# Performance work log

Measured on AMD Instinct MI355X. Metric: run time of the kernel, lower is better.

## Reference

```python
import jax, jax.numpy as jnp
import numpy as np
from jax import lax

B, C_IN, C_OUT, N, R, K = 16, 64, 64, 32768, 32, 3
GROUPS, GN_EPS = 8, 1e-5


def swish(x):
    return x * jax.nn.sigmoid(x)


def group_norm(x, gamma, beta):
    b, c = x.shape[:2]
    xg = x.reshape(b, GROUPS, -1)
    mu = xg.mean(-1, keepdims=True)
    var = xg.var(-1, keepdims=True)
    xn = ((xg - mu) * lax.rsqrt(var + GN_EPS)).reshape(x.shape)
    shp = (1, c) + (1,) * (x.ndim - 2)
    return xn * gamma.reshape(shp) + beta.reshape(shp)


def conv3d(x, w, b):
    y = lax.conv_general_dilated(x, w, (1, 1, 1), 'SAME',
                                 dimension_numbers=('NCDHW', 'OIDHW', 'NCDHW'))
    return y + b.reshape(1, -1, 1, 1, 1)


def voxelize(features, coords):
    # features [B,C,N], coords [B,3,N] -> vox [B,C,R,R,R], norm_coords [B,3,N] in [0,R-1]
    c = coords - coords.mean(axis=2, keepdims=True)
    scale = jnp.linalg.norm(c, axis=1, keepdims=True).max(axis=2, keepdims=True) * 2.0  # eps=0
    norm = jnp.clip((c / scale + 0.5) * R, 0.0, R - 1)
    vc = jnp.round(norm).astype(jnp.int32)
    idx = (vc[:, 0] * R + vc[:, 1]) * R + vc[:, 2]  # [B,N] flat voxel index

    def per_batch(f, i):  # f [C,N], i [N] -> [C, R^3] scatter-average
        sums = jax.ops.segment_sum(f.T, i, num_segments=R ** 3)  # [R^3, C]
        cnt = jax.ops.segment_sum(jnp.ones(i.shape, f.dtype), i, num_segments=R ** 3)
        return (sums / jnp.maximum(cnt, 1.0)[:, None]).T

    vox = jax.vmap(per_batch)(features, idx).reshape(features.shape[0], features.shape[1], R, R, R)
    return vox, norm


def trilinear_devoxelize(vox, coords):
    # vox [B,C,R,R,R], coords [B,3,N] float in [0,R-1] -> [B,C,N]
    b, c = vox.shape[:2]
    flat = vox.reshape(b, c, R ** 3)
    c0f = jnp.floor(coords)
    f = coords - c0f
    i0 = jnp.clip(c0f.astype(jnp.int32), 0, R - 1)
    i1 = jnp.clip(i0 + 1, 0, R - 1)
    out = jnp.zeros((b, c, coords.shape[2]), vox.dtype)
    for xi, wx in ((i0[:, 0], 1.0 - f[:, 0]), (i1[:, 0], f[:, 0])):
        for yi, wy in ((i0[:, 1], 1.0 - f[:, 1]), (i1[:, 1], f[:, 1])):
            for zi, wz in ((i0[:, 2], 1.0 - f[:, 2]), (i1[:, 2], f[:, 2])):
                idx = (xi * R + yi) * R + zi  # [B,N]
                w = (wx * wy * wz)[:, None, :]
                out = out + jnp.take_along_axis(flat, idx[:, None, :], axis=2) * w
    return out


def setup_inputs():
    key = jax.random.key(0)
    ks = jax.random.split(key, 6)
    s1 = 1.0 / np.sqrt(C_IN * K ** 3)
    s2 = 1.0 / np.sqrt(C_OUT * K ** 3)
    sp = 1.0 / np.sqrt(C_IN)
    return {
        'features': jax.random.normal(ks[0], (B, C_IN, N), jnp.float32),
        'coords': jax.random.normal(ks[1], (B, 3, N), jnp.float32),
        'w1': jax.random.normal(ks[2], (C_OUT, C_IN, K, K, K), jnp.float32) * s1,
        'b1': jnp.zeros((C_OUT,), jnp.float32),
        'g1': jnp.ones((C_OUT,), jnp.float32),
        'be1': jnp.zeros((C_OUT,), jnp.float32),
        'w2': jax.random.normal(ks[3], (C_OUT, C_OUT, K, K, K), jnp.float32) * s2,
        'b2': jnp.zeros((C_OUT,), jnp.float32),
        'g2': jnp.ones((C_OUT,), jnp.float32),
        'be2': jnp.zeros((C_OUT,), jnp.float32),
        'wp': jax.random.normal(ks[4], (C_OUT, C_IN), jnp.float32) * sp,
        'bp': jnp.zeros((C_OUT,), jnp.float32),
        'gp': jnp.ones((C_OUT,), jnp.float32),
        'bep': jnp.zeros((C_OUT,), jnp.float32),
    }


def reference(features, coords, w1, b1, g1, be1, w2, b2, g2, be2, wp, bp, gp, bep):
    coords_sg = lax.stop_gradient(coords)  # torch: coords.detach() inside Voxelization
    vox, norm_coords = voxelize(features, coords_sg)
    h = swish(group_norm(conv3d(vox, w1, b1), g1, be1))
    # Dropout(0.1) is identity in eval mode
    h = swish(group_norm(conv3d(h, w2, b2), g2, be2))
    vpts = trilinear_devoxelize(h, norm_coords)
    pf = swish(group_norm(jnp.einsum('oc,bcn->bon', wp, features) + bp[None, :, None], gp, bep))
    return (vpts + pf, coords)
```

## Files before the change

kernel.cpp:

```cpp
#include <hip/hip_runtime.h>
#include <hip/hip_bf16.h>
#include <math.h>

#define BB   16
#define CCH  64
#define NPT  32768
#define RR   32
#define R3   32768
#define GSZ  262144
#define VOXB 2228224

typedef __attribute__((ext_vector_type(8))) short bfx8;
typedef __attribute__((ext_vector_type(8))) unsigned short usx8;
typedef __attribute__((ext_vector_type(16))) float f32x16;

__device__ __forceinline__ short f2bf(float f) {
    unsigned u = __builtin_bit_cast(unsigned, f);
    u += 0x7fff + ((u >> 16) & 1);
    return (short)(u >> 16);
}
__device__ __forceinline__ float bf2f(unsigned short s) {
    unsigned u = ((unsigned)s) << 16;
    return __builtin_bit_cast(float, u);
}

__device__ __forceinline__ float blockReduceSumF(float v) {
    __shared__ float sm[16];
    #pragma unroll
    for (int o = 32; o > 0; o >>= 1) v += __shfl_down(v, o);
    __syncthreads();
    if ((threadIdx.x & 63) == 0) sm[threadIdx.x >> 6] = v;
    __syncthreads();
    float s = 0.f;
    int nw = blockDim.x >> 6;
    for (int i = 0; i < nw; ++i) s += sm[i];
    return s;
}

__device__ __forceinline__ float blockReduceMaxF(float v) {
    __shared__ float sm[16];
    #pragma unroll
    for (int o = 32; o > 0; o >>= 1) v = fmaxf(v, __shfl_down(v, o));
    __syncthreads();
    if ((threadIdx.x & 63) == 0) sm[threadIdx.x >> 6] = v;
    __syncthreads();
    float s = sm[0];
    int nw = blockDim.x >> 6;
    for (int i = 1; i < nw; ++i) s = fmaxf(s, sm[i]);
    return s;
}

__global__ void k_cstat_sum(const float* __restrict__ coords, float* __restrict__ csum) {
    int b = blockIdx.x >> 3, seg = blockIdx.x & 7;
    const float* cb = coords + (size_t)b * 3 * NPT;
    int n0 = seg << 12;
    float sx = 0.f, sy = 0.f, sz = 0.f;
    for (int n = n0 + threadIdx.x; n < n0 + 4096; n += 256) {
        sx += cb[n]; sy += cb[NPT + n]; sz += cb[2 * NPT + n];
    }
    sx = blockReduceSumF(sx);
    sy = blockReduceSumF(sy);
    sz = blockReduceSumF(sz);
    if (threadIdx.x == 0) {
        atomicAdd(&csum[b * 4 + 0], sx);
        atomicAdd(&csum[b * 4 + 1], sy);
        atomicAdd(&csum[b * 4 + 2], sz);
    }
}

__global__ void k_cstat_max(const float* __restrict__ coords, const float* __restrict__ csum,
                            int* __restrict__ cmax) {
    int b = blockIdx.x >> 3, seg = blockIdx.x & 7;
    const float* cb = coords + (size_t)b * 3 * NPT;
    float mx = csum[b * 4 + 0] * (1.f / NPT);
    float my = csum[b * 4 + 1] * (1.f / NPT);
    float mz = csum[b * 4 + 2] * (1.f / NPT);
    int n0 = seg << 12;
    float mn = 0.f;
    for (int n = n0 + threadIdx.x; n < n0 + 4096; n += 256) {
        float x = cb[n] - mx, y = cb[NPT + n] - my, z = cb[2 * NPT + n] - mz;
        mn = fmaxf(mn, sqrtf(x * x + y * y + z * z));
    }
    mn = blockReduceMaxF(mn);
    if (threadIdx.x == 0) atomicMax(&cmax[b], __float_as_int(mn));
}

__global__ void k_norm_idx(const float* __restrict__ coords, const float* __restrict__ csum,
                           const int* __restrict__ cmax,
                           float* __restrict__ normc, int* __restrict__ vidx,
                           int* __restrict__ hist, float* __restrict__ out2) {
    int t = blockIdx.x * 256 + threadIdx.x;
    int b = t >> 15, n = t & 32767;
    float mx = csum[b * 4 + 0] * (1.f / NPT);
    float my = csum[b * 4 + 1] * (1.f / NPT);
    float mz = csum[b * 4 + 2] * (1.f / NPT);
    float scale = 2.f * __int_as_float(cmax[b]);
    const float* cb = coords + (size_t)b * 3 * NPT;
    float x = cb[n], y = cb[NPT + n], z = cb[2 * NPT + n];
    float nx = fminf(fmaxf(((x - mx) / scale + 0.5f) * 32.f, 0.f), 31.f);
    float ny = fminf(fmaxf(((y - my) / scale + 0.5f) * 32.f, 0.f), 31.f);
    float nz = fminf(fmaxf(((z - mz) / scale + 0.5f) * 32.f, 0.f), 31.f);
    float* nb = normc + (size_t)b * 3 * NPT;
    nb[n] = nx; nb[NPT + n] = ny; nb[2 * NPT + n] = nz;
    int vx = (int)rintf(nx), vy = (int)rintf(ny), vz = (int)rintf(nz);
    int v = (vx * 32 + vy) * 32 + vz;
    vidx[t] = v;
    atomicAdd(&hist[(b << 15) + v], 1);
    float* o2 = out2 + (size_t)b * 3 * NPT;
    o2[n] = x; o2[NPT + n] = y; o2[2 * NPT + n] = z;
}

__global__ __launch_bounds__(1024) void k_prefix(const int* __restrict__ hist,
                                                 int* __restrict__ startB,
                                                 int* __restrict__ base) {
    int b = blockIdx.x;
    int tid = threadIdx.x;
    const int* h = hist + (b << 15);
    int loc[32];
    int s = 0;
    #pragma unroll
    for (int j = 0; j < 32; ++j) { loc[j] = h[tid * 32 + j]; s += loc[j]; }
    __shared__ int sm[1024];
    sm[tid] = s;
    __syncthreads();
    for (int o = 1; o < 1024; o <<= 1) {
        int v = (tid >= o) ? sm[tid - o] : 0;
        __syncthreads();
        sm[tid] += v;
        __syncthreads();
    }
    int run = (tid ? sm[tid - 1] : 0);
    #pragma unroll
    for (int j = 0; j < 32; ++j) {
        int idx = (b << 15) + tid * 32 + j;
        startB[idx] = run;
        base[idx] = run;
        run += loc[j];
    }
}

__global__ __launch_bounds__(256) void k_reorder(const float* __restrict__ feat,
                                                 const int* __restrict__ vidx,
                                                 int* __restrict__ base,
                                                 short* __restrict__ featT) {
    __shared__ float tile[64][65];
    __shared__ int sslot[64];
    int blk = blockIdx.x;
    int b = blk >> 9;
    int n0 = (blk & 511) << 6;
    int tid = threadIdx.x;
    const float* fb = feat + ((size_t)b << 21);
    for (int e = tid; e < 64 * 64; e += 256) {
        int c = e >> 6, nn = e & 63;
        tile[c][nn] = fb[((size_t)c << 15) + n0 + nn];
    }
    if (tid < 64) {
        int v = vidx[(b << 15) + n0 + tid];
        sslot[tid] = atomicAdd(&base[(b << 15) + v], 1);
    }
    __syncthreads();
    int p = tid >> 2, q = tid & 3;
    int slot = sslot[p];
    short* dst = featT + (((size_t)((b << 15) + slot)) << 6) + q * 16;
    unsigned pk[8];
    #pragma unroll
    for (int k = 0; k < 8; ++k) {
        unsigned lo16 = (unsigned short)f2bf(tile[q * 16 + 2 * k][p]);
        unsigned hi16 = (unsigned short)f2bf(tile[q * 16 + 2 * k + 1][p]);
        pk[k] = lo16 | (hi16 << 16);
    }
    *(int4*)dst = make_int4(pk[0], pk[1], pk[2], pk[3]);
    *(int4*)(dst + 8) = make_int4(pk[4], pk[5], pk[6], pk[7]);
}

__global__ void k_vox_accum(const short* __restrict__ featT, const int* __restrict__ startB,
                            const int* __restrict__ base, short* __restrict__ vout) {
    int t = blockIdx.x * 256 + threadIdx.x;
    int lane4 = t & 15;
    int v = (t >> 4) & 32767;
    int b = t >> 19;
    int start = startB[(b << 15) + v];
    int end   = base[(b << 15) + v];
    float4 acc = make_float4(0.f, 0.f, 0.f, 0.f);
    const short* fT = featT + (((size_t)b << 15) << 6) + lane4 * 4;
    for (int p = start; p < end; ++p) {
        short4 hv = *(const short4*)(fT + ((size_t)p << 6));
        acc.x += bf2f((unsigned short)hv.x);
        acc.y += bf2f((unsigned short)hv.y);
        acc.z += bf2f((unsigned short)hv.z);
        acc.w += bf2f((unsigned short)hv.w);
    }
    float rc = 1.f / fmaxf((float)(end - start), 1.f);
    short4 pk;
    pk.x = f2bf(acc.x * rc); pk.y = f2bf(acc.y * rc);
    pk.z = f2bf(acc.z * rc); pk.w = f2bf(acc.w * rc);
    *(short4*)(vout + (size_t)b * VOXB + ((size_t)(v >> 5) * 34 + (v & 31) + 1) * 64 + lane4 * 4) = pk;
}

__global__ void k_padzero(short* __restrict__ v) {
    int t = blockIdx.x * 256 + threadIdx.x;
    int q = t & 7, zp = (t >> 3) & 1, xy = (t >> 4) & 1023, b = t >> 14;
    int z = zp ? 33 : 0;
    *(int4*)(v + (size_t)b * VOXB + ((size_t)xy * 34 + z) * 64 + q * 8) = make_int4(0, 0, 0, 0);
}

__global__ void k_wprep(const float* __restrict__ w, short* __restrict__ wT) {
    int e = blockIdx.x * 256 + threadIdx.x;
    int ci = e & 63, co = (e >> 6) & 63, k = e >> 12;
    wT[e] = f2bf(w[(size_t)(co * 64 + ci) * 27 + k]);
}

__global__ __launch_bounds__(256, 2) void k_conv_mfma(
    const short* __restrict__ vin, const short* __restrict__ wT,
    const float* __restrict__ bias, short* __restrict__ vout, float* __restrict__ st)
{
    __shared__ short lds[36 * 1088];
    __shared__ float sred[8][2];
    int bid = blockIdx.x;
    int xcd = bid & 7, sub = bid >> 3;
    int b = (xcd << 1) | (sub >> 6);
    int tile = sub & 63;
    int x0 = (tile >> 3) << 2, y0 = (tile & 7) << 2;
    int tid = threadIdx.x;
    int wv = tid >> 6, l = tid & 63;
    int lo = l & 31, hi = l >> 5;
    const short* vb = vin + (size_t)b * VOXB;
    int xo = x0 + wv;
    if (tid < 16) ((float*)sred)[tid] = 0.f;

    f32x16 acc[2][4];
    #pragma unroll
    for (int cb = 0; cb < 2; ++cb)
        #pragma unroll
        for (int j = 0; j < 4; ++j)
            #pragma unroll
            for (int i = 0; i < 16; ++i) acc[cb][j][i] = 0.f;

    #pragma unroll
    for (int h = 0; h < 2; ++h) {
        if (h) __syncthreads();
        for (int e = tid; e < 4896; e += 256) {
            int line = e / 136, r = e - line * 136;
            int z = r >> 2, q = r & 3;
            int xx = line / 6, yy = line - xx * 6;
            int xi = x0 + xx - 1, yi = y0 + yy - 1;
            int4 v = make_int4(0, 0, 0, 0);
            if ((unsigned)xi < 32u && (unsigned)yi < 32u)
                v = *(const int4*)(vb + ((size_t)(xi * 32 + yi) * 34 + z) * 64 + h * 32 + q * 8);
            int dst = line * 1088 + z * 32 + ((q * 8) ^ ((z & 3) << 3));
            *(int4*)(lds + dst) = v;
        }
        __syncthreads();
        const short* wbase = wT + lo * 64 + h * 32 + hi * 8;
        #pragma unroll
        for (int dx = 0; dx < 3; ++dx) {
            const short* ldsx = lds + ((wv + dx) * 6) * 1088;
            #pragma unroll
            for (int dz = 0; dz < 3; ++dz) {
                int zz = lo + dz;
                int swz = (zz & 3) << 3;
                const short* bcol = ldsx + zz * 32;
                #pragma unroll
                for (int s = 0; s < 2; ++s) {
                    int slot = (s * 16 + hi * 8) ^ swz;
                    const short* wt0 = wbase + (dx * 9 + dz) * 4096 + s * 16;
                    bfx8 wA0 = *(const bfx8*)(wt0);
                    bfx8 wB0 = *(const bfx8*)(wt0 + 2048);
                    bfx8 wA1 = *(const bfx8*)(wt0 + 3 * 4096);
                    bfx8 wB1 = *(const bfx8*)(wt0 + 3 * 4096 + 2048);
                    bfx8 wA2 = *(const bfx8*)(wt0 + 6 * 4096);
                    bfx8 wB2 = *(const bfx8*)(wt0 + 6 * 4096 + 2048);
                    #pragma unroll
                    for (int L = 0; L < 6; ++L) {
                        bfx8 bv = *(const bfx8*)(bcol + L * 1088 + slot);
                        if (L <= 3) {
                            acc[0][L] = __builtin_amdgcn_mfma_f32_32x32x16_bf16(wA0, bv, acc[0][L], 0, 0, 0);
                            acc[1][L] = __builtin_amdgcn_mfma_f32_32x32x16_bf16(wB0, bv, acc[1][L], 0, 0, 0);
                        }
                        if (L >= 1 && L <= 4) {
                            acc[0][L-1] = __builtin_amdgcn_mfma_f32_32x32x16_bf16(wA1, bv, acc[0][L-1], 0, 0, 0);
                            acc[1][L-1] = __builtin_amdgcn_mfma_f32_32x32x16_bf16(wB1, bv, acc[1][L-1], 0, 0, 0);
                        }
                        if (L >= 2) {
                            acc[0][L-2] = __builtin_amdgcn_mfma_f32_32x32x16_bf16(wA2, bv, acc[0][L-2], 0, 0, 0);
                            acc[1][L-2] = __builtin_amdgcn_mfma_f32_32x32x16_bf16(wB2, bv, acc[1][L-2], 0, 0, 0);
                        }
                    }
                }
            }
        }
    }

    float gs[8], gs2[8];
    #pragma unroll
    for (int g = 0; g < 8; ++g) { gs[g] = 0.f; gs2[g] = 0.f; }
    short* ob = vout + (size_t)b * VOXB;
    #pragma unroll
    for (int cb = 0; cb < 2; ++cb) {
        #pragma unroll
        for (int j = 0; j < 4; ++j) {
            size_t rb = ((size_t)(xo * 32 + y0 + j) * 34 + 1 + lo) * 64;
            #pragma unroll
            for (int q = 0; q < 4; ++q) {
                int co0 = cb * 32 + hi * 4 + q * 8;
                float v0 = acc[cb][j][q * 4 + 0] + bias[co0 + 0];
                float v1 = acc[cb][j][q * 4 + 1] + bias[co0 + 1];
                float v2 = acc[cb][j][q * 4 + 2] + bias[co0 + 2];
                float v3 = acc[cb][j][q * 4 + 3] + bias[co0 + 3];
                int g = cb * 4 + q;
                gs[g] += v0 + v1 + v2 + v3;
                gs2[g] += v0 * v0 + v1 * v1 + v2 * v2 + v3 * v3;
                short4 pk;
                pk.x = f2bf(v0); pk.y = f2bf(v1); pk.z = f2bf(v2); pk.w = f2bf(v3);
                *(short4*)(ob + rb + co0) = pk;
            }
        }
    }
    #pragma unroll
    for (int g = 0; g < 8; ++g) {
        float s = gs[g], s2 = gs2[g];
        #pragma unroll
        for (int o = 32; o > 0; o >>= 1) { s += __shfl_down(s, o); s2 += __shfl_down(s2, o); }
        if (l == 0) { atomicAdd(&sred[g][0], s); atomicAdd(&sred[g][1], s2); }
    }
    __syncthreads();
    if (tid < 8) {
        atomicAdd(&st[((b << 3) + tid) * 2 + 0], sred[tid][0]);
        atomicAdd(&st[((b << 3) + tid) * 2 + 1], sred[tid][1]);
    }
}

__global__ void k_gn_apply_b(short* __restrict__ v, const float* __restrict__ st,
                             const float* __restrict__ gamma, const float* __restrict__ beta) {
    int e = blockIdx.x * 256 + threadIdx.x;
    int cg = e & 7, vx = (e >> 3) & 32767, b = e >> 18;
    float s = st[(b * 8 + cg) * 2 + 0], s2 = st[(b * 8 + cg) * 2 + 1];
    float mean = s * (1.f / 262144.f);
    float var = s2 * (1.f / 262144.f) - mean * mean;
    float rstd = rsqrtf(var + 1e-5f);
    short* p = v + (size_t)b * VOXB + ((size_t)(vx >> 5) * 34 + (vx & 31) + 1) * 64 + cg * 8;
    usx8 hv = *(const usx8*)p;
    usx8 ov;
    #pragma unroll
    for (int i = 0; i < 8; ++i) {
        int co = cg * 8 + i;
        float f = bf2f(hv[i]);
        float g = (f - mean) * rstd * gamma[co] + beta[co];
        float sw = g / (1.f + __expf(-g));
        ov[i] = (unsigned short)f2bf(sw);
    }
    *(usx8*)p = ov;
}

__global__ __launch_bounds__(256) void k_point(const float* __restrict__ feat,
                                               const float* __restrict__ wp,
                                               const float* __restrict__ bp,
                                               short* __restrict__ pbuf,
                                               float* __restrict__ stp) {
    __shared__ float s_f[64][64];
    __shared__ float s_w[64][68];
    __shared__ float sred[8][2];
    int nblk = blockIdx.x * 64;
    int b = blockIdx.y;
    int tid = threadIdx.x;
    if (tid < 16) ((float*)sred)[tid] = 0.f;
    const float* fb = feat + (((size_t)b * CCH) << 15);
    for (int e = tid; e < 64 * 64; e += 256) {
        int c = e >> 6, nn = e & 63;
        s_f[c][nn] = fb[(((size_t)c) << 15) + nblk + nn];
        s_w[nn][c] = wp[e];
    }
    __syncthreads();
    int o0 = (tid >> 4) << 2;
    int n0 = (tid & 15) << 2;
    float acc[4][4] = {{0.f}};
    for (int c = 0; c < 64; ++c) {
        float4 fv = *(const float4*)&s_f[c][n0];
        float4 wv = *(const float4*)&s_w[c][o0];
        float fvv[4] = {fv.x, fv.y, fv.z, fv.w};
        float wvv[4] = {wv.x, wv.y, wv.z, wv.w};
        #pragma unroll
        for (int j = 0; j < 4; ++j)
            #pragma unroll
            for (int i = 0; i < 4; ++i) acc[j][i] += wvv[j] * fvv[i];
    }
    float s = 0.f, s2 = 0.f;
    #pragma unroll
    for (int j = 0; j < 4; ++j) {
        float bb = bp[o0 + j];
        short* op = pbuf + (((size_t)(b * CCH + o0 + j)) << 15) + nblk + n0;
        short4 pk;
        float v0 = acc[j][0] + bb, v1 = acc[j][1] + bb;
        float v2 = acc[j][2] + bb, v3 = acc[j][3] + bb;
        s += v0 + v1 + v2 + v3;
        s2 += v0 * v0 + v1 * v1 + v2 * v2 + v3 * v3;
        pk.x = f2bf(v0); pk.y = f2bf(v1); pk.z = f2bf(v2); pk.w = f2bf(v3);
        *(short4*)op = pk;
    }
    int g = o0 >> 3;
    atomicAdd(&sred[g][0], s);
    atomicAdd(&sred[g][1], s2);
    __syncthreads();
    if (tid < 8) {
        atomicAdd(&stp[(b * 8 + tid) * 2 + 0], sred[tid][0]);
        atomicAdd(&stp[(b * 8 + tid) * 2 + 1], sred[tid][1]);
    }
}

__global__ void k_final(const short* __restrict__ h, const float* __restrict__ normc,
                        const float* __restrict__ stp, const float* __restrict__ gp,
                        const float* __restrict__ bep, const short* __restrict__ pbuf,
                        float* __restrict__ out1) {
    int tid = threadIdx.x;
    int s = tid & 7, pp = tid >> 3;
    int pt = blockIdx.x * 32 + pp;
    int b = pt >> 15, n = pt & 32767;
    const float* nb = normc + (size_t)b * 3 * NPT;
    float nx = nb[n], ny = nb[NPT + n], nz = nb[2 * NPT + n];
    float fxf = floorf(nx), fyf = floorf(ny), fzf = floorf(nz);
    float fx = nx - fxf, fy = ny - fyf, fz = nz - fzf;
    int x0 = (int)fxf; x0 = x0 < 31 ? x0 : 31;
    int y0 = (int)fyf; y0 = y0 < 31 ? y0 : 31;
    int z0 = (int)fzf; z0 = z0 < 31 ? z0 : 31;
    int x1 = x0 + 1 < 31 ? x0 + 1 : 31;
    int y1 = y0 + 1 < 31 ? y0 + 1 : 31;
    int z1 = z0 + 1 < 31 ? z0 + 1 : 31;
    float wx0 = 1.f - fx, wx1 = fx, wy0 = 1.f - fy, wy1 = fy, wz0 = 1.f - fz, wz1 = fz;
    const short* hb = h + (size_t)b * VOXB + s * 8;
    float acc[8];
    #pragma unroll
    for (int i = 0; i < 8; ++i) acc[i] = 0.f;
    #pragma unroll
    for (int cx = 0; cx < 2; ++cx) {
        int xi = cx ? x1 : x0; float wxx = cx ? wx1 : wx0;
        #pragma unroll
        for (int cy = 0; cy < 2; ++cy) {
            int yi = cy ? y1 : y0; float wyy = cy ? wy1 : wy0;
            #pragma unroll
            for (int cz = 0; cz < 2; ++cz) {
                int zi = cz ? z1 : z0; float wzz = cz ? wz1 : wz0;
                float w = wxx * wyy * wzz;
                usx8 hv = *(const usx8*)(hb + ((size_t)(xi * 32 + yi) * 34 + zi + 1) * 64);
                #pragma unroll
                for (int i = 0; i < 8; ++i) acc[i] = fmaf(w, bf2f(hv[i]), acc[i]);
            }
        }
    }
    float ss = stp[(b * 8 + s) * 2 + 0], ss2 = stp[(b * 8 + s) * 2 + 1];
    float mean = ss * (1.f / 262144.f);
    float rstd = rsqrtf(ss2 * (1.f / 262144.f) - mean * mean + 1e-5f);
    const short* pb = pbuf + (((size_t)(b * CCH)) << 15) + n;
    #pragma unroll
    for (int i = 0; i < 8; ++i) {
        int co = s * 8 + i;
        float* op = out1 + (((size_t)(b * CCH + co)) << 15) + n;
        float pv = bf2f((unsigned short)pb[((size_t)co) << 15]);
        float g = (pv - mean) * rstd * gp[co] + bep[co];
        float sw = g / (1.f + __expf(-g));
        *op = acc[i] + sw;
    }
}

extern "C" void kernel_launch(void* const* d_in, const int* in_sizes, int n_in,
                              void* d_out, int out_size, void* d_ws, size_t ws_size,
                              hipStream_t stream) {
    const float* feat   = (const float*)d_in[0];
    const float* coords = (const float*)d_in[1];
    const float* w1  = (const float*)d_in[2];
    const float* b1  = (const float*)d_in[3];
    const float* g1  = (const float*)d_in[4];
    const float* be1 = (const float*)d_in[5];
    const float* w2  = (const float*)d_in[6];
    const float* b2  = (const float*)d_in[7];
    const float* g2  = (const float*)d_in[8];
    const float* be2 = (const float*)d_in[9];
    const float* wp  = (const float*)d_in[10];
    const float* bp  = (const float*)d_in[11];
    const float* gp  = (const float*)d_in[12];
    const float* bep = (const float*)d_in[13];

    float* out1 = (float*)d_out;
    float* out2 = out1 + (size_t)BB * CCH * NPT;

    const size_t reg0Bytes = (size_t)BB * NPT * CCH * 4;
    short* featT    = (short*)d_ws;
    short* voxT_mid = (short*)d_ws;
    short* pbuf     = (short*)d_ws;
    short* voxT_in  = (short*)((char*)d_ws + reg0Bytes);
    char* p = (char*)voxT_in + (size_t)BB * VOXB * 2;
    int*   hist   = (int*)p;  p += (size_t)BB * R3 * 4;
    int*   startB = (int*)p;  p += (size_t)BB * R3 * 4;
    int*   base   = (int*)p;  p += (size_t)BB * R3 * 4;
    float* normc = (float*)p; p += (size_t)BB * 3 * NPT * 4;
    int*   vidx  = (int*)p;   p += (size_t)BB * NPT * 4;
    short* wT1   = (short*)p; p += 110592 * 2;
    short* wT2   = (short*)p; p += 110592 * 2;
    float* st1   = (float*)p; p += 256 * 4;
    float* st2   = (float*)p; p += 256 * 4;
    float* stp   = (float*)p; p += 256 * 4;
    float* csum  = (float*)p; p += 64 * 4;
    int*   cmax  = (int*)p;   p += 16 * 4;

    hipMemsetAsync(hist, 0, (size_t)BB * R3 * 4, stream);
    hipMemsetAsync(st1, 0, (256 * 3 + 64 + 16) * 4, stream);

    k_padzero<<<1024, 256, 0, stream>>>(voxT_in);
    k_cstat_sum<<<128, 256, 0, stream>>>(coords, csum);
    k_cstat_max<<<128, 256, 0, stream>>>(coords, csum, cmax);
    k_norm_idx<<<(BB * NPT) / 256, 256, 0, stream>>>(coords, csum, cmax, normc, vidx, hist, out2);
    k_prefix<<<BB, 1024, 0, stream>>>(hist, startB, base);
    k_reorder<<<(BB * NPT) / 64, 256, 0, stream>>>(feat, vidx, base, featT);
    k_vox_accum<<<(BB * R3 * 16) / 256, 256, 0, stream>>>(featT, startB, base, voxT_in);
    k_wprep<<<432, 256, 0, stream>>>(w1, wT1);
    k_wprep<<<432, 256, 0, stream>>>(w2, wT2);

    k_padzero<<<1024, 256, 0, stream>>>(voxT_mid);

    k_conv_mfma<<<1024, 256, 0, stream>>>(voxT_in, wT1, b1, voxT_mid, st1);
    k_gn_apply_b<<<(BB * R3 * 8) / 256, 256, 0, stream>>>(voxT_mid, st1, g1, be1);

    k_conv_mfma<<<1024, 256, 0, stream>>>(voxT_mid, wT2, b2, voxT_in, st2);
    k_gn_apply_b<<<(BB * R3 * 8) / 256, 256, 0, stream>>>(voxT_in, st2, g2, be2);

    k_point<<<dim3(NPT / 64, BB), 256, 0, stream>>>(feat, wp, bp, pbuf, stp);

    k_final<<<(BB * NPT) / 32, 256, 0, stream>>>(voxT_in, normc, stp, gp, bep, pbuf, out1);
}
```

Before: 745.1 us.

## Fuse first GroupNorm+swish into second conv load, split output channels across 8 waves

The first GroupNorm-apply and swish pass is folded into the second conv's LDS staging loop, so the standalone normalize kernel over the intermediate volume goes away. The conv now runs 512 threads per block, with each wave owning one 32-channel half. That halves accumulator registers per wave and raises occupancy. The reorder kernel's feature tile load is also vectorised to float4. In exchange, the fused path recomputes the per-group stats and gamma/beta for every staged element, and adds exp work to the load phase.

```diff
diff --git a/kernel.cpp b/kernel.cpp
--- a/kernel.cpp
+++ b/kernel.cpp
@@ -150,9 +150,11 @@
     int n0 = (blk & 511) << 6;
     int tid = threadIdx.x;
     const float* fb = feat + ((size_t)b << 21);
-    for (int e = tid; e < 64 * 64; e += 256) {
-        int c = e >> 6, nn = e & 63;
-        tile[c][nn] = fb[((size_t)c << 15) + n0 + nn];
+    for (int e = tid; e < 64 * 16; e += 256) {
+        int c = e >> 4, n4 = e & 15;
+        float4 v4 = *(const float4*)(fb + ((size_t)c << 15) + n0 + n4 * 4);
+        tile[c][n4 * 4 + 0] = v4.x; tile[c][n4 * 4 + 1] = v4.y;
+        tile[c][n4 * 4 + 2] = v4.z; tile[c][n4 * 4 + 3] = v4.w;
     }
     if (tid < 64) {
         int v = vidx[(b << 15) + n0 + tid];
@@ -210,9 +212,13 @@
     wT[e] = f2bf(w[(size_t)(co * 64 + ci) * 27 + k]);
 }
 
-__global__ __launch_bounds__(256, 2) void k_conv_mfma(
+template<bool FUSE>
+__global__ __launch_bounds__(512, 4) void k_conv_mfma(
     const short* __restrict__ vin, const short* __restrict__ wT,
-    const float* __restrict__ bias, short* __restrict__ vout, float* __restrict__ st)
+    const float* __restrict__ bias,
+    const float* __restrict__ stin, const float* __restrict__ gin,
+    const float* __restrict__ bein,
+    short* __restrict__ vout, float* __restrict__ st)
 {
     __shared__ short lds[36 * 1088];
     __shared__ float sred[8][2];
@@ -222,39 +228,62 @@
     int tile = sub & 63;
     int x0 = (tile >> 3) << 2, y0 = (tile & 7) << 2;
     int tid = threadIdx.x;
-    int wv = tid >> 6, l = tid & 63;
-    int lo = l & 31, hi = l >> 5;
+    int wv8 = tid >> 6;
+    int cb = wv8 & 1, xl = wv8 >> 1;
+    int l = tid & 63, lo = l & 31, hi = l >> 5;
     const short* vb = vin + (size_t)b * VOXB;
-    int xo = x0 + wv;
+    int xo = x0 + xl;
     if (tid < 16) ((float*)sred)[tid] = 0.f;
 
-    f32x16 acc[2][4];
-    #pragma unroll
-    for (int cb = 0; cb < 2; ++cb)
+    f32x16 acc[4];
+    #pragma unroll
+    for (int j = 0; j < 4; ++j)
         #pragma unroll
-        for (int j = 0; j < 4; ++j)
-            #pragma unroll
-            for (int i = 0; i < 16; ++i) acc[cb][j][i] = 0.f;
+        for (int i = 0; i < 16; ++i) acc[j][i] = 0.f;
 
     #pragma unroll
     for (int h = 0; h < 2; ++h) {
         if (h) __syncthreads();
-        for (int e = tid; e < 4896; e += 256) {
+        for (int e = tid; e < 4896; e += 512) {
             int line = e / 136, r = e - line * 136;
             int z = r >> 2, q = r & 3;
             int xx = line / 6, yy = line - xx * 6;
             int xi = x0 + xx - 1, yi = y0 + yy - 1;
+            bool inb = ((unsigned)xi < 32u) && ((unsigned)yi < 32u);
             int4 v = make_int4(0, 0, 0, 0);
-            if ((unsigned)xi < 32u && (unsigned)yi < 32u)
+            if (inb)
                 v = *(const int4*)(vb + ((size_t)(xi * 32 + yi) * 34 + z) * 64 + h * 32 + q * 8);
+            if (FUSE) {
+                if (inb && z >= 1 && z <= 32) {
+                    int ci0 = h * 32 + q * 8, cg = ci0 >> 3;
+                    float s = stin[((b << 3) + cg) * 2 + 0];
+                    float s2 = stin[((b << 3) + cg) * 2 + 1];
+                    float mean = s * (1.f / 262144.f);
+                    float rstd = rsqrtf(s2 * (1.f / 262144.f) - mean * mean + 1e-5f);
+                    float4 ga = *(const float4*)(gin + ci0);
+                    float4 gb = *(const float4*)(gin + ci0 + 4);
+                    float4 ba = *(const float4*)(bein + ci0);
+                    float4 bb = *(const float4*)(bein + ci0 + 4);
+                    float gm[8] = {ga.x, ga.y, ga.z, ga.w, gb.x, gb.y, gb.z, gb.w};
+                    float bt[8] = {ba.x, ba.y, ba.z, ba.w, bb.x, bb.y, bb.z, bb.w};
+                    unsigned short* hv = (unsigned short*)&v;
+                    #pragma unroll
+                    for (int i = 0; i < 8; ++i) {
+                        float f = bf2f(hv[i]);
+                        float g = (f - mean) * rstd * gm[i] + bt[i];
+                        float sw = g / (1.f + __expf(-g));
+                        hv[i] = (unsigned short)f2bf(sw);
+                    }
+                }
+            }
             int dst = line * 1088 + z * 32 + ((q * 8) ^ ((z & 3) << 3));
             *(int4*)(lds + dst) = v;
         }
         __syncthreads();
-        const short* wbase = wT + lo * 64 + h * 32 + hi * 8;
+        const short* wbase = wT + lo * 64 + h * 32 + hi * 8 + cb * 2048;
         #pragma unroll
         for (int dx = 0; dx < 3; ++dx) {
-            const short* ldsx = lds + ((wv + dx) * 6) * 1088;
+            const short* ldsx = lds + ((xl + dx) * 6) * 1088;
             #pragma unroll
             for (int dz = 0; dz < 3; ++dz) {
                 int zz = lo + dz;
@@ -264,64 +293,51 @@
                 for (int s = 0; s < 2; ++s) {
                     int slot = (s * 16 + hi * 8) ^ swz;
                     const short* wt0 = wbase + (dx * 9 + dz) * 4096 + s * 16;
-                    bfx8 wA0 = *(const bfx8*)(wt0);
-                    bfx8 wB0 = *(const bfx8*)(wt0 + 2048);
-                    bfx8 wA1 = *(const bfx8*)(wt0 + 3 * 4096);
-                    bfx8 wB1 = *(const bfx8*)(wt0 + 3 * 4096 + 2048);
-                    bfx8 wA2 = *(const bfx8*)(wt0 + 6 * 4096);
-                    bfx8 wB2 = *(const bfx8*)(wt0 + 6 * 4096 + 2048);
+                    bfx8 w0 = *(const bfx8*)(wt0);
+                    bfx8 w1 = *(const bfx8*)(wt0 + 3 * 4096);
+                    bfx8 w2 = *(const bfx8*)(wt0 + 6 * 4096);
                     #pragma unroll
                     for (int L = 0; L < 6; ++L) {
                         bfx8 bv = *(const bfx8*)(bcol + L * 1088 + slot);
-                        if (L <= 3) {
-                            acc[0][L] = __builtin_amdgcn_mfma_f32_32x32x16_bf16(wA0, bv, acc[0][L], 0, 0, 0);
-                            acc[1][L] = __builtin_amdgcn_mfma_f32_32x32x16_bf16(wB0, bv, acc[1][L], 0, 0, 0);
-                        }
-                        if (L >= 1 && L <= 4) {
-                            acc[0][L-1] = __builtin_amdgcn_mfma_f32_32x32x16_bf16(wA1, bv, acc[0][L-1], 0, 0, 0);
-                            acc[1][L-1] = __builtin_amdgcn_mfma_f32_32x32x16_bf16(wB1, bv, acc[1][L-1], 0, 0, 0);
-                        }
-                        if (L >= 2) {
-                            acc[0][L-2] = __builtin_amdgcn_mfma_f32_32x32x16_bf16(wA2, bv, acc[0][L-2], 0, 0, 0);
-                            acc[1][L-2] = __builtin_amdgcn_mfma_f32_32x32x16_bf16(wB2, bv, acc[1][L-2], 0, 0, 0);
-                        }
+                        if (L <= 3)
+                            acc[L] = __builtin_amdgcn_mfma_f32_32x32x16_bf16(w0, bv, acc[L], 0, 0, 0);
+                        if (L >= 1 && L <= 4)
+                            acc[L-1] = __builtin_amdgcn_mfma_f32_32x32x16_bf16(w1, bv, acc[L-1], 0, 0, 0);
+                        if (L >= 2)
+                            acc[L-2] = __builtin_amdgcn_mfma_f32_32x32x16_bf16(w2, bv, acc[L-2], 0, 0, 0);
                     }
                 }
             }
         }
     }
 
-    float gs[8], gs2[8];
-    #pragma unroll
-    for (int g = 0; g < 8; ++g) { gs[g] = 0.f; gs2[g] = 0.f; }
+    float gs[4], gs2[4];
+    #pragma unroll
+    for (int g = 0; g < 4; ++g) { gs[g] = 0.f; gs2[g] = 0.f; }
     short* ob = vout + (size_t)b * VOXB;
     #pragma unroll
-    for (int cb = 0; cb < 2; ++cb) {
+    for (int j = 0; j < 4; ++j) {
+        size_t rb = ((size_t)(xo * 32 + y0 + j) * 34 + 1 + lo) * 64;
         #pragma unroll
-        for (int j = 0; j < 4; ++j) {
-            size_t rb = ((size_t)(xo * 32 + y0 + j) * 34 + 1 + lo) * 64;
-            #pragma unroll
-            for (int q = 0; q < 4; ++q) {
-                int co0 = cb * 32 + hi * 4 + q * 8;
-                float v0 = acc[cb][j][q * 4 + 0] + bias[co0 + 0];
-                float v1 = acc[cb][j][q * 4 + 1] + bias[co0 + 1];
-                float v2 = acc[cb][j][q * 4 + 2] + bias[co0 + 2];
-                float v3 = acc[cb][j][q * 4 + 3] + bias[co0 + 3];
-                int g = cb * 4 + q;
-                gs[g] += v0 + v1 + v2 + v3;
-                gs2[g] += v0 * v0 + v1 * v1 + v2 * v2 + v3 * v3;
-                short4 pk;
-                pk.x = f2bf(v0); pk.y = f2bf(v1); pk.z = f2bf(v2); pk.w = f2bf(v3);
-                *(short4*)(ob + rb + co0) = pk;
-            }
+        for (int q = 0; q < 4; ++q) {
+            int co0 = cb * 32 + hi * 4 + q * 8;
+            float v0 = acc[j][q * 4 + 0] + bias[co0 + 0];
+            float v1 = acc[j][q * 4 + 1] + bias[co0 + 1];
+            float v2 = acc[j][q * 4 + 2] + bias[co0 + 2];
+            float v3 = acc[j][q * 4 + 3] + bias[co0 + 3];
+            gs[q] += v0 + v1 + v2 + v3;
+            gs2[q] += v0 * v0 + v1 * v1 + v2 * v2 + v3 * v3;
+            short4 pk;
+            pk.x = f2bf(v0); pk.y = f2bf(v1); pk.z = f2bf(v2); pk.w = f2bf(v3);
+            *(short4*)(ob + rb + co0) = pk;
         }
     }
     #pragma unroll
-    for (int g = 0; g < 8; ++g) {
-        float s = gs[g], s2 = gs2[g];
+    for (int q = 0; q < 4; ++q) {
+        float s = gs[q], s2 = gs2[q];
         #pragma unroll
         for (int o = 32; o > 0; o >>= 1) { s += __shfl_down(s, o); s2 += __shfl_down(s2, o); }
-        if (l == 0) { atomicAdd(&sred[g][0], s); atomicAdd(&sred[g][1], s2); }
+        if (l == 0) { atomicAdd(&sred[cb * 4 + q][0], s); atomicAdd(&sred[cb * 4 + q][1], s2); }
     }
     __syncthreads();
     if (tid < 8) {
@@ -516,10 +532,10 @@
 
     k_padzero<<<1024, 256, 0, stream>>>(voxT_mid);
 
-    k_conv_mfma<<<1024, 256, 0, stream>>>(voxT_in, wT1, b1, voxT_mid, st1);
-    k_gn_apply_b<<<(BB * R3 * 8) / 256, 256, 0, stream>>>(voxT_mid, st1, g1, be1);
-
-    k_conv_mfma<<<1024, 256, 0, stream>>>(voxT_mid, wT2, b2, voxT_in, st2);
+    k_conv_mfma<false><<<1024, 512, 0, stream>>>(voxT_in, wT1, b1,
+                                                 nullptr, nullptr, nullptr, voxT_mid, st1);
+    k_conv_mfma<true><<<1024, 512, 0, stream>>>(voxT_mid, wT2, b2,
+                                                st1, g1, be1, voxT_in, st2);
     k_gn_apply_b<<<(BB * R3 * 8) / 256, 256, 0, stream>>>(voxT_in, st2, g2, be2);
 
     k_point<<<dim3(NPT / 64, BB), 256, 0, stream>>>(feat, wp, bp, pbuf, stp);
```

After: 720.2 us. 1.03x faster.

## Fuse GroupNorm+swish into conv2 load and devoxelize; vectorize reorder loads

Applied to the files above, without the earlier changes.

Removes both standalone GroupNorm-apply passes over the voxel grid. The first GN+swish is now applied while conv2 stages its input tiles into LDS, with padding and out-of-bounds voxels kept at zero. The second is applied per gathered corner inside the final trilinear kernel. The LDS swizzle gains an extra XOR term to reduce bank conflicts, and the reorder kernel loads features as float4. In exchange, the swish is recomputed for every halo load in conv2 and for all 8 corners per point in the final kernel, adding exp work in place of two memory passes.

```diff
diff --git a/kernel.cpp b/kernel.cpp
--- a/kernel.cpp
+++ b/kernel.cpp
@@ -22,6 +22,10 @@
 __device__ __forceinline__ float bf2f(unsigned short s) {
     unsigned u = ((unsigned)s) << 16;
     return __builtin_bit_cast(float, u);
+}
+
+__device__ __forceinline__ int fzswz(int z) {
+    return (((z & 3) ^ ((z >> 2) & 3)) << 3);
 }
 
 __device__ __forceinline__ float blockReduceSumF(float v) {
@@ -150,9 +154,11 @@
     int n0 = (blk & 511) << 6;
     int tid = threadIdx.x;
     const float* fb = feat + ((size_t)b << 21);
-    for (int e = tid; e < 64 * 64; e += 256) {
-        int c = e >> 6, nn = e & 63;
-        tile[c][nn] = fb[((size_t)c << 15) + n0 + nn];
+    for (int e = tid; e < 64 * 16; e += 256) {
+        int c = e >> 4, n4 = e & 15;
+        float4 v4 = *(const float4*)(fb + ((size_t)c << 15) + n0 + n4 * 4);
+        tile[c][n4 * 4 + 0] = v4.x; tile[c][n4 * 4 + 1] = v4.y;
+        tile[c][n4 * 4 + 2] = v4.z; tile[c][n4 * 4 + 3] = v4.w;
     }
     if (tid < 64) {
         int v = vidx[(b << 15) + n0 + tid];
@@ -210,9 +216,13 @@
     wT[e] = f2bf(w[(size_t)(co * 64 + ci) * 27 + k]);
 }
 
+template<bool FUSE>
 __global__ __launch_bounds__(256, 2) void k_conv_mfma(
     const short* __restrict__ vin, const short* __restrict__ wT,
-    const float* __restrict__ bias, short* __restrict__ vout, float* __restrict__ st)
+    const float* __restrict__ bias,
+    const float* __restrict__ stin, const float* __restrict__ gin,
+    const float* __restrict__ bein,
+    short* __restrict__ vout, float* __restrict__ st)
 {
     __shared__ short lds[36 * 1088];
     __shared__ float sred[8][2];
@@ -244,10 +254,34 @@
             int z = r >> 2, q = r & 3;
             int xx = line / 6, yy = line - xx * 6;
             int xi = x0 + xx - 1, yi = y0 + yy - 1;
+            bool inb = ((unsigned)xi < 32u) && ((unsigned)yi < 32u);
             int4 v = make_int4(0, 0, 0, 0);
-            if ((unsigned)xi < 32u && (unsigned)yi < 32u)
+            if (inb)
                 v = *(const int4*)(vb + ((size_t)(xi * 32 + yi) * 34 + z) * 64 + h * 32 + q * 8);
-            int dst = line * 1088 + z * 32 + ((q * 8) ^ ((z & 3) << 3));
+            if (FUSE) {
+                if (inb && z >= 1 && z <= 32) {
+                    int ci0 = h * 32 + q * 8, cg = ci0 >> 3;
+                    float s = stin[((b << 3) + cg) * 2 + 0];
+                    float s2 = stin[((b << 3) + cg) * 2 + 1];
+                    float mean = s * (1.f / 262144.f);
+                    float rstd = rsqrtf(s2 * (1.f / 262144.f) - mean * mean + 1e-5f);
+                    float4 ga = *(const float4*)(gin + ci0);
+                    float4 gb = *(const float4*)(gin + ci0 + 4);
+                    float4 ba = *(const float4*)(bein + ci0);
+                    float4 bb = *(const float4*)(bein + ci0 + 4);
+                    float gm[8] = {ga.x, ga.y, ga.z, ga.w, gb.x, gb.y, gb.z, gb.w};
+                    float bt[8] = {ba.x, ba.y, ba.z, ba.w, bb.x, bb.y, bb.z, bb.w};
+                    unsigned short* hv = (unsigned short*)&v;
+                    #pragma unroll
+                    for (int i = 0; i < 8; ++i) {
+                        float f = bf2f(hv[i]);
+                        float g = (f - mean) * rstd * gm[i] + bt[i];
+                        float sw = g / (1.f + __expf(-g));
+                        hv[i] = (unsigned short)f2bf(sw);
+                    }
+                }
+            }
+            int dst = line * 1088 + z * 32 + ((q * 8) ^ fzswz(z));
             *(int4*)(lds + dst) = v;
         }
         __syncthreads();
@@ -258,7 +292,7 @@
             #pragma unroll
             for (int dz = 0; dz < 3; ++dz) {
                 int zz = lo + dz;
-                int swz = (zz & 3) << 3;
+                int swz = fzswz(zz);
                 const short* bcol = ldsx + zz * 32;
                 #pragma unroll
                 for (int s = 0; s < 2; ++s) {
@@ -330,28 +364,6 @@
     }
 }
 
-__global__ void k_gn_apply_b(short* __restrict__ v, const float* __restrict__ st,
-                             const float* __restrict__ gamma, const float* __restrict__ beta) {
-    int e = blockIdx.x * 256 + threadIdx.x;
-    int cg = e & 7, vx = (e >> 3) & 32767, b = e >> 18;
-    float s = st[(b * 8 + cg) * 2 + 0], s2 = st[(b * 8 + cg) * 2 + 1];
-    float mean = s * (1.f / 262144.f);
-    float var = s2 * (1.f / 262144.f) - mean * mean;
-    float rstd = rsqrtf(var + 1e-5f);
-    short* p = v + (size_t)b * VOXB + ((size_t)(vx >> 5) * 34 + (vx & 31) + 1) * 64 + cg * 8;
-    usx8 hv = *(const usx8*)p;
-    usx8 ov;
-    #pragma unroll
-    for (int i = 0; i < 8; ++i) {
-        int co = cg * 8 + i;
-        float f = bf2f(hv[i]);
-        float g = (f - mean) * rstd * gamma[co] + beta[co];
-        float sw = g / (1.f + __expf(-g));
-        ov[i] = (unsigned short)f2bf(sw);
-    }
-    *(usx8*)p = ov;
-}
-
 __global__ __launch_bounds__(256) void k_point(const float* __restrict__ feat,
                                                const float* __restrict__ wp,
                                                const float* __restrict__ bp,
@@ -408,6 +420,8 @@
 }
 
 __global__ void k_final(const short* __restrict__ h, const float* __restrict__ normc,
+                        const float* __restrict__ st2, const float* __restrict__ g2v,
+                        const float* __restrict__ be2v,
                         const float* __restrict__ stp, const float* __restrict__ gp,
                         const float* __restrict__ bep, const short* __restrict__ pbuf,
                         float* __restrict__ out1) {
@@ -426,6 +440,18 @@
     int y1 = y0 + 1 < 31 ? y0 + 1 : 31;
     int z1 = z0 + 1 < 31 ? z0 + 1 : 31;
     float wx0 = 1.f - fx, wx1 = fx, wy0 = 1.f - fy, wy1 = fy, wz0 = 1.f - fz, wz1 = fz;
+
+    float s2m = st2[(b * 8 + s) * 2 + 0], s2q = st2[(b * 8 + s) * 2 + 1];
+    float mean2 = s2m * (1.f / 262144.f);
+    float rstd2 = rsqrtf(s2q * (1.f / 262144.f) - mean2 * mean2 + 1e-5f);
+    float scl[8], sft[8];
+    #pragma unroll
+    for (int i = 0; i < 8; ++i) {
+        float gmm = g2v[s * 8 + i];
+        scl[i] = gmm * rstd2;
+        sft[i] = be2v[s * 8 + i] - mean2 * gmm * rstd2;
+    }
+
     const short* hb = h + (size_t)b * VOXB + s * 8;
     float acc[8];
     #pragma unroll
@@ -442,7 +468,11 @@
                 float w = wxx * wyy * wzz;
                 usx8 hv = *(const usx8*)(hb + ((size_t)(xi * 32 + yi) * 34 + zi + 1) * 64);
                 #pragma unroll
-                for (int i = 0; i < 8; ++i) acc[i] = fmaf(w, bf2f(hv[i]), acc[i]);
+                for (int i = 0; i < 8; ++i) {
+                    float g = bf2f(hv[i]) * scl[i] + sft[i];
+                    float sw = g / (1.f + __expf(-g));
+                    acc[i] = fmaf(w, sw, acc[i]);
+                }
             }
         }
     }
@@ -516,13 +546,13 @@
 
     k_padzero<<<1024, 256, 0, stream>>>(voxT_mid);
 
-    k_conv_mfma<<<1024, 256, 0, stream>>>(voxT_in, wT1, b1, voxT_mid, st1);
-    k_gn_apply_b<<<(BB * R3 * 8) / 256, 256, 0, stream>>>(voxT_mid, st1, g1, be1);
-
-    k_conv_mfma<<<1024, 256, 0, stream>>>(voxT_mid, wT2, b2, voxT_in, st2);
-    k_gn_apply_b<<<(BB * R3 * 8) / 256, 256, 0, stream>>>(voxT_in, st2, g2, be2);
+    k_conv_mfma<false><<<1024, 256, 0, stream>>>(voxT_in, wT1, b1,
+                                                 nullptr, nullptr, nullptr, voxT_mid, st1);
+    k_conv_mfma<true><<<1024, 256, 0, stream>>>(voxT_mid, wT2, b2,
+                                                st1, g1, be1, voxT_in, st2);
 
     k_point<<<dim3(NPT / 64, BB), 256, 0, stream>>>(feat, wp, bp, pbuf, stp);
 
-    k_final<<<(BB * NPT) / 32, 256, 0, stream>>>(voxT_in, normc, stp, gp, bep, pbuf, out1);
-}
+    k_final<<<(BB * NPT) / 32, 256, 0, stream>>>(voxT_in, normc, st2, g2, be2,
+                                                 stp, gp, bep, pbuf, out1);
+}
```

After: 787.3 us. 5.7% more time.
